# Kernel optimization log

Measured on AMD Instinct MI355X. Metric: run time of the kernel, lower is better.

The kernel has to match this reference:

```python
import jax, jax.numpy as jnp
import numpy as np

B, S, D, U = 64, 2048, 512, 512

def setup_inputs() -> dict:
    key = jax.random.key(0)
    ks = jax.random.split(key, 8)
    query = jax.random.normal(ks[0], (B, D), dtype=jnp.float32)
    values = jax.random.normal(ks[1], (B, S, D), dtype=jnp.float32)
    # Keras Dense params (glorot-like scale), with biases (Dense default use_bias=True)
    W1 = jax.random.normal(ks[2], (D, U), dtype=jnp.float32) / np.sqrt(D)
    b1 = jnp.zeros((U,), dtype=jnp.float32)
    W2 = jax.random.normal(ks[3], (D, U), dtype=jnp.float32) / np.sqrt(D)
    b2 = jnp.zeros((U,), dtype=jnp.float32)
    V = jax.random.normal(ks[4], (U, 1), dtype=jnp.float32) / np.sqrt(U)
    bv = jnp.zeros((1,), dtype=jnp.float32)
    return {"query": query, "values": values, "W1": W1, "b1": b1,
            "W2": W2, "b2": b2, "V": V, "bv": bv}

def reference(query, values, W1, b1, W2, b2, V, bv) -> jnp.ndarray:
    # query: [B, D], values: [B, S, D]
    q_proj = query @ W1 + b1                      # [B, U]
    v_proj = jnp.einsum('bsd,du->bsu', values, W2) + b2  # [B, S, U]
    h = jnp.tanh(q_proj[:, None, :] + v_proj)     # [B, S, U]
    scores = jnp.einsum('bsu,uo->bso', h, V) + bv # [B, S, 1]
    attn = jax.nn.softmax(scores, axis=1)         # softmax over sequence axis
    context = jnp.sum(attn * values, axis=1)      # [B, D]
    return context
```

## Files before the change

kernel.cpp:

```cpp
#include <hip/hip_runtime.h>
#include <hip/hip_bf16.h>

#define BB 64
#define SS 2048
#define DD 512
#define UU 512
#define BS (BB*SS)

typedef __attribute__((ext_vector_type(8))) short bf16x8;
typedef __attribute__((ext_vector_type(4))) float f32x4;

static __device__ __forceinline__ unsigned short f2bf(float x) {
    union { float f; unsigned int u; } v; v.f = x;
    unsigned int r = v.u + 0x7FFFu + ((v.u >> 16) & 1u);
    return (unsigned short)(r >> 16);
}

__global__ void k_w2t(const float* __restrict__ W2, unsigned short* __restrict__ W2T) {
    __shared__ float tile[64][65];
    const int ti = blockIdx.x >> 3;
    const int tj = blockIdx.x & 7;
    const int t = threadIdx.x;
    #pragma unroll
    for (int i = 0; i < 16; ++i) {
        int e = i*256 + t;
        int dr = e >> 6, uc = e & 63;
        tile[dr][uc] = W2[(size_t)(ti*64+dr)*UU + tj*64+uc];
    }
    __syncthreads();
    #pragma unroll
    for (int i = 0; i < 16; ++i) {
        int e = i*256 + t;
        int ur = e >> 6, dc = e & 63;
        W2T[(size_t)(tj*64+ur)*DD + ti*64+dc] = f2bf(tile[dc][ur]);
    }
}

__global__ void k_qproj(const float* __restrict__ query, const float* __restrict__ W1,
                        const float* __restrict__ b1, const float* __restrict__ b2,
                        float* __restrict__ qpb) {
    const int b = blockIdx.x, t = threadIdx.x;
    float a0 = 0.f, a1 = 0.f;
    for (int d = 0; d < DD; ++d) {
        float q = query[b*DD + d];
        a0 += q * W1[(size_t)d*UU + t];
        a1 += q * W1[(size_t)d*UU + t + 256];
    }
    qpb[b*UU + t]       = a0 + b1[t]     + b2[t];
    qpb[b*UU + t + 256] = a1 + b1[t+256] + b2[t+256];
}

__launch_bounds__(256, 2)
__global__ void k_scores(const float* __restrict__ values,
                         const unsigned short* __restrict__ W2T,
                         const float* __restrict__ qpb,
                         const float* __restrict__ Vw,
                         float* __restrict__ scores) {
    __shared__ unsigned short Albuf[64*512];
    const int t  = threadIdx.x;
    const int m0 = blockIdx.x * 64;
    const int b  = m0 >> 11;

    const float* src = values + (size_t)m0 * DD;
    #pragma unroll
    for (int i = 0; i < 16; ++i) {
        int gf  = i*256 + t;
        int row = gf >> 6;
        int g   = gf & 63;
        const float4 f0 = *(const float4*)(src + (size_t)row*DD + g*8);
        const float4 f1 = *(const float4*)(src + (size_t)row*DD + g*8 + 4);
        ushort4 lo, hi;
        lo.x = f2bf(f0.x); lo.y = f2bf(f0.y); lo.z = f2bf(f0.z); lo.w = f2bf(f0.w);
        hi.x = f2bf(f1.x); hi.y = f2bf(f1.y); hi.z = f2bf(f1.z); hi.w = f2bf(f1.w);
        int gs = g ^ (row & 7);
        ushort4* dst = (ushort4*)&Albuf[row*512 + gs*8];
        dst[0] = lo; dst[1] = hi;
    }
    __syncthreads();

    const int wave = t >> 6, lane = t & 63;
    const int ln15 = lane & 15, quad = lane >> 4;

    float sacc[4][4] = {};

    for (int nc = 0; nc < 2; ++nc) {
        const int nwb = nc*256 + wave*64;
        f32x4 acc[4][4];
        #pragma unroll
        for (int mt = 0; mt < 4; ++mt)
            #pragma unroll
            for (int nt = 0; nt < 4; ++nt)
                acc[mt][nt] = f32x4{0.f, 0.f, 0.f, 0.f};

        #pragma unroll 2
        for (int k0 = 0; k0 < DD; k0 += 32) {
            const int kq = k0 + quad*8;
            bf16x8 bfr[4], afr[4];
            #pragma unroll
            for (int nt = 0; nt < 4; ++nt) {
                int n = nwb + nt*16 + ln15;
                bfr[nt] = *(const bf16x8*)(W2T + (size_t)n*DD + kq);
            }
            #pragma unroll
            for (int mt = 0; mt < 4; ++mt) {
                int m = mt*16 + ln15;
                int g = (kq >> 3) ^ (m & 7);
                afr[mt] = *(const bf16x8*)&Albuf[m*512 + g*8];
            }
            #pragma unroll
            for (int mt = 0; mt < 4; ++mt)
                #pragma unroll
                for (int nt = 0; nt < 4; ++nt)
                    acc[mt][nt] = __builtin_amdgcn_mfma_f32_16x16x32_bf16(
                        afr[mt], bfr[nt], acc[mt][nt], 0, 0, 0);
        }

        #pragma unroll
        for (int nt = 0; nt < 4; ++nt) {
            int n = nwb + nt*16 + ln15;
            float qv = qpb[b*UU + n];
            float vw = Vw[n];
            #pragma unroll
            for (int mt = 0; mt < 4; ++mt)
                #pragma unroll
                for (int r = 0; r < 4; ++r) {
                    float x = qv + acc[mt][nt][r];
                    float e = __expf(x + x);
                    float h = 1.f - 2.f / (e + 1.f);
                    sacc[mt][r] += h * vw;
                }
        }
    }

    #pragma unroll
    for (int mt = 0; mt < 4; ++mt)
        #pragma unroll
        for (int r = 0; r < 4; ++r) {
            float v = sacc[mt][r];
            v += __shfl_xor(v, 1);
            v += __shfl_xor(v, 2);
            v += __shfl_xor(v, 4);
            v += __shfl_xor(v, 8);
            if (ln15 == 0)
                atomicAdd(&scores[m0 + mt*16 + quad*4 + r], v);
        }
}

__global__ void k_softmax(const float* __restrict__ scores, float* __restrict__ wts) {
    __shared__ float red[64];
    const int b = blockIdx.x, t = threadIdx.x;
    const float* s = scores + b*SS;
    float v[8];
    float mx = -1e30f;
    #pragma unroll
    for (int i = 0; i < 8; ++i) { v[i] = s[i*256 + t]; mx = fmaxf(mx, v[i]); }
    #pragma unroll
    for (int off = 32; off; off >>= 1) mx = fmaxf(mx, __shfl_xor(mx, off));
    if ((t & 63) == 0) red[t >> 6] = mx;
    __syncthreads();
    mx = fmaxf(fmaxf(red[0], red[1]), fmaxf(red[2], red[3]));
    float sum = 0.f;
    #pragma unroll
    for (int i = 0; i < 8; ++i) { v[i] = __expf(v[i] - mx); sum += v[i]; }
    #pragma unroll
    for (int off = 32; off; off >>= 1) sum += __shfl_xor(sum, off);
    __syncthreads();
    if ((t & 63) == 0) red[t >> 6] = sum;
    __syncthreads();
    sum = red[0] + red[1] + red[2] + red[3];
    float inv = 1.f / sum;
    #pragma unroll
    for (int i = 0; i < 8; ++i) wts[b*SS + i*256 + t] = v[i] * inv;
}

__launch_bounds__(256)
__global__ void k_context(const float* __restrict__ values, const float* __restrict__ wts,
                          float* __restrict__ out) {
    __shared__ float4 red[16][16];
    const int blk = blockIdx.x;
    const int b = blk >> 3, d0 = (blk & 7) * 64;
    const int t = threadIdx.x;
    const int di = t & 15, sg = t >> 4;
    float4 acc = make_float4(0.f, 0.f, 0.f, 0.f);
    const float* vb = values + (size_t)b*SS*DD + d0 + di*4;
    const float* wb = wts + b*SS;
    #pragma unroll 4
    for (int s = sg; s < SS; s += 16) {
        float w = wb[s];
        float4 v = *(const float4*)(vb + (size_t)s*DD);
        acc.x += w*v.x; acc.y += w*v.y; acc.z += w*v.z; acc.w += w*v.w;
    }
    red[sg][di] = acc;
    __syncthreads();
    if (t < 16) {
        float4 sum = make_float4(0.f, 0.f, 0.f, 0.f);
        #pragma unroll
        for (int g = 0; g < 16; ++g) {
            float4 v = red[g][t];
            sum.x += v.x; sum.y += v.y; sum.z += v.z; sum.w += v.w;
        }
        *(float4*)(out + (size_t)b*DD + d0 + t*4) = sum;
    }
}

extern "C" void kernel_launch(void* const* d_in, const int* in_sizes, int n_in,
                              void* d_out, int out_size, void* d_ws, size_t ws_size,
                              hipStream_t stream) {
    const float* query  = (const float*)d_in[0];
    const float* values = (const float*)d_in[1];
    const float* W1     = (const float*)d_in[2];
    const float* b1     = (const float*)d_in[3];
    const float* W2     = (const float*)d_in[4];
    const float* b2     = (const float*)d_in[5];
    const float* Vw     = (const float*)d_in[6];

    char* ws = (char*)d_ws;
    unsigned short* W2T = (unsigned short*)ws;
    float* qpb    = (float*)(ws + 524288);
    float* scores = (float*)(ws + 524288 + 131072);
    float* wts    = (float*)(ws + 524288 + 131072 + 524288);
    float* out    = (float*)d_out;

    hipMemsetAsync(scores, 0, BS * sizeof(float), stream);
    k_w2t<<<64, 256, 0, stream>>>(W2, W2T);
    k_qproj<<<BB, 256, 0, stream>>>(query, W1, b1, b2, qpb);
    k_scores<<<BS/64, 256, 0, stream>>>(values, W2T, qpb, Vw, scores);
    k_softmax<<<BB, 256, 0, stream>>>(scores, wts);
    k_context<<<BB*8, 256, 0, stream>>>(values, wts, out);
}
```

Baseline: 576.1 us.

## Merge prep kernels, fuse softmax into context, prefetch W2T, drop atomics

Merges the W2 transpose and query-projection kernels into one launch. Folds the softmax into the context kernel, so each block recomputes the per-batch softmax and keeps the weights in shared memory. In the scores kernel, W2T fragments are now double-buffered in registers and the per-column q/V constants are hoisted. The atomic score accumulation is replaced by a shared-memory reduction with a plain store, which removes the memset. Softmax work is repeated 8 times per batch, and register pressure in the scores kernel goes up.

```diff
diff --git a/kernel.cpp b/kernel.cpp
--- a/kernel.cpp
+++ b/kernel.cpp
@@ -16,38 +16,39 @@
     return (unsigned short)(r >> 16);
 }
 
-__global__ void k_w2t(const float* __restrict__ W2, unsigned short* __restrict__ W2T) {
+__global__ void k_prep(const float* __restrict__ W2, unsigned short* __restrict__ W2T,
+                       const float* __restrict__ query, const float* __restrict__ W1,
+                       const float* __restrict__ b1, const float* __restrict__ b2,
+                       float* __restrict__ qpb) {
     __shared__ float tile[64][65];
-    const int ti = blockIdx.x >> 3;
-    const int tj = blockIdx.x & 7;
     const int t = threadIdx.x;
-    #pragma unroll
-    for (int i = 0; i < 16; ++i) {
-        int e = i*256 + t;
-        int dr = e >> 6, uc = e & 63;
-        tile[dr][uc] = W2[(size_t)(ti*64+dr)*UU + tj*64+uc];
-    }
-    __syncthreads();
-    #pragma unroll
-    for (int i = 0; i < 16; ++i) {
-        int e = i*256 + t;
-        int ur = e >> 6, dc = e & 63;
-        W2T[(size_t)(tj*64+ur)*DD + ti*64+dc] = f2bf(tile[dc][ur]);
-    }
-}
-
-__global__ void k_qproj(const float* __restrict__ query, const float* __restrict__ W1,
-                        const float* __restrict__ b1, const float* __restrict__ b2,
-                        float* __restrict__ qpb) {
-    const int b = blockIdx.x, t = threadIdx.x;
-    float a0 = 0.f, a1 = 0.f;
-    for (int d = 0; d < DD; ++d) {
-        float q = query[b*DD + d];
-        a0 += q * W1[(size_t)d*UU + t];
-        a1 += q * W1[(size_t)d*UU + t + 256];
-    }
-    qpb[b*UU + t]       = a0 + b1[t]     + b2[t];
-    qpb[b*UU + t + 256] = a1 + b1[t+256] + b2[t+256];
+    if (blockIdx.x < 64) {
+        const int ti = blockIdx.x >> 3;
+        const int tj = blockIdx.x & 7;
+        #pragma unroll
+        for (int i = 0; i < 16; ++i) {
+            int e = i*256 + t;
+            int dr = e >> 6, uc = e & 63;
+            tile[dr][uc] = W2[(size_t)(ti*64+dr)*UU + tj*64+uc];
+        }
+        __syncthreads();
+        #pragma unroll
+        for (int i = 0; i < 16; ++i) {
+            int e = i*256 + t;
+            int ur = e >> 6, dc = e & 63;
+            W2T[(size_t)(tj*64+ur)*DD + ti*64+dc] = f2bf(tile[dc][ur]);
+        }
+    } else {
+        const int b = blockIdx.x - 64;
+        float a0 = 0.f, a1 = 0.f;
+        for (int d = 0; d < DD; ++d) {
+            float q = query[b*DD + d];
+            a0 += q * W1[(size_t)d*UU + t];
+            a1 += q * W1[(size_t)d*UU + t + 256];
+        }
+        qpb[b*UU + t]       = a0 + b1[t]     + b2[t];
+        qpb[b*UU + t + 256] = a1 + b1[t+256] + b2[t+256];
+    }
 }
 
 __launch_bounds__(256, 2)
@@ -60,6 +61,19 @@
     const int t  = threadIdx.x;
     const int m0 = blockIdx.x * 64;
     const int b  = m0 >> 11;
+
+    const int wave = t >> 6, lane = t & 63;
+    const int ln15 = lane & 15, quad = lane >> 4;
+
+    float qv[2][4], vw[2][4];
+    #pragma unroll
+    for (int nc = 0; nc < 2; ++nc)
+        #pragma unroll
+        for (int nt = 0; nt < 4; ++nt) {
+            int n = nc*256 + wave*64 + nt*16 + ln15;
+            qv[nc][nt] = qpb[b*UU + n];
+            vw[nc][nt] = Vw[n];
+        }
 
     const float* src = values + (size_t)m0 * DD;
     #pragma unroll
@@ -78,13 +92,25 @@
     }
     __syncthreads();
 
-    const int wave = t >> 6, lane = t & 63;
-    const int ln15 = lane & 15, quad = lane >> 4;
+    const unsigned short* bp[4];
+    #pragma unroll
+    for (int nt = 0; nt < 4; ++nt)
+        bp[nt] = W2T + (size_t)(wave*64 + nt*16 + ln15) * DD + quad*8;
+
+    int abase[4];
+    #pragma unroll
+    for (int mt = 0; mt < 4; ++mt)
+        abase[mt] = (mt*16 + ln15) * 512;
+    const int xm = ln15 & 7;
 
     float sacc[4][4] = {};
 
+    bf16x8 bb[2][4];
+    #pragma unroll
+    for (int nt = 0; nt < 4; ++nt)
+        bb[0][nt] = *(const bf16x8*)(bp[nt]);
+
     for (int nc = 0; nc < 2; ++nc) {
-        const int nwb = nc*256 + wave*64;
         f32x4 acc[4][4];
         #pragma unroll
         for (int mt = 0; mt < 4; ++mt)
@@ -92,46 +118,48 @@
             for (int nt = 0; nt < 4; ++nt)
                 acc[mt][nt] = f32x4{0.f, 0.f, 0.f, 0.f};
 
-        #pragma unroll 2
-        for (int k0 = 0; k0 < DD; k0 += 32) {
-            const int kq = k0 + quad*8;
-            bf16x8 bfr[4], afr[4];
-            #pragma unroll
-            for (int nt = 0; nt < 4; ++nt) {
-                int n = nwb + nt*16 + ln15;
-                bfr[nt] = *(const bf16x8*)(W2T + (size_t)n*DD + kq);
+        #pragma unroll
+        for (int ks = 0; ks < 16; ++ks) {
+            const int j   = nc*16 + ks;
+            const int cur = j & 1;
+            if (j + 1 < 32) {
+                const int jn  = j + 1;
+                const int off = (jn >> 4) * (256*DD) + (jn & 15) * 32;
+                #pragma unroll
+                for (int nt = 0; nt < 4; ++nt)
+                    bb[cur ^ 1][nt] = *(const bf16x8*)(bp[nt] + off);
             }
-            #pragma unroll
-            for (int mt = 0; mt < 4; ++mt) {
-                int m = mt*16 + ln15;
-                int g = (kq >> 3) ^ (m & 7);
-                afr[mt] = *(const bf16x8*)&Albuf[m*512 + g*8];
-            }
+            bf16x8 afr[4];
+            const int g4 = ks*4 + quad;
+            #pragma unroll
+            for (int mt = 0; mt < 4; ++mt)
+                afr[mt] = *(const bf16x8*)&Albuf[abase[mt] + ((g4 ^ xm) << 3)];
             #pragma unroll
             for (int mt = 0; mt < 4; ++mt)
                 #pragma unroll
                 for (int nt = 0; nt < 4; ++nt)
                     acc[mt][nt] = __builtin_amdgcn_mfma_f32_16x16x32_bf16(
-                        afr[mt], bfr[nt], acc[mt][nt], 0, 0, 0);
+                        afr[mt], bb[cur][nt], acc[mt][nt], 0, 0, 0);
         }
 
         #pragma unroll
         for (int nt = 0; nt < 4; ++nt) {
-            int n = nwb + nt*16 + ln15;
-            float qv = qpb[b*UU + n];
-            float vw = Vw[n];
+            const float q = qv[nc][nt];
+            const float w = vw[nc][nt];
             #pragma unroll
             for (int mt = 0; mt < 4; ++mt)
                 #pragma unroll
                 for (int r = 0; r < 4; ++r) {
-                    float x = qv + acc[mt][nt][r];
+                    float x = q + acc[mt][nt][r];
                     float e = __expf(x + x);
-                    float h = 1.f - 2.f / (e + 1.f);
-                    sacc[mt][r] += h * vw;
+                    float rc = __builtin_amdgcn_rcpf(e + 1.f);
+                    sacc[mt][r] = fmaf(fmaf(-2.f, rc, 1.f), w, sacc[mt][r]);
                 }
         }
     }
 
+    __syncthreads();
+    float* buf = (float*)Albuf;
     #pragma unroll
     for (int mt = 0; mt < 4; ++mt)
         #pragma unroll
@@ -141,65 +169,66 @@
             v += __shfl_xor(v, 2);
             v += __shfl_xor(v, 4);
             v += __shfl_xor(v, 8);
-            if (ln15 == 0)
-                atomicAdd(&scores[m0 + mt*16 + quad*4 + r], v);
-        }
-}
-
-__global__ void k_softmax(const float* __restrict__ scores, float* __restrict__ wts) {
-    __shared__ float red[64];
-    const int b = blockIdx.x, t = threadIdx.x;
-    const float* s = scores + b*SS;
-    float v[8];
-    float mx = -1e30f;
-    #pragma unroll
-    for (int i = 0; i < 8; ++i) { v[i] = s[i*256 + t]; mx = fmaxf(mx, v[i]); }
-    #pragma unroll
-    for (int off = 32; off; off >>= 1) mx = fmaxf(mx, __shfl_xor(mx, off));
-    if ((t & 63) == 0) red[t >> 6] = mx;
-    __syncthreads();
-    mx = fmaxf(fmaxf(red[0], red[1]), fmaxf(red[2], red[3]));
-    float sum = 0.f;
-    #pragma unroll
-    for (int i = 0; i < 8; ++i) { v[i] = __expf(v[i] - mx); sum += v[i]; }
-    #pragma unroll
-    for (int off = 32; off; off >>= 1) sum += __shfl_xor(sum, off);
-    __syncthreads();
-    if ((t & 63) == 0) red[t >> 6] = sum;
-    __syncthreads();
-    sum = red[0] + red[1] + red[2] + red[3];
-    float inv = 1.f / sum;
-    #pragma unroll
-    for (int i = 0; i < 8; ++i) wts[b*SS + i*256 + t] = v[i] * inv;
+            if (ln15 == 0) buf[wave*64 + mt*16 + quad*4 + r] = v;
+        }
+    __syncthreads();
+    if (t < 64)
+        scores[m0 + t] = buf[t] + buf[64 + t] + buf[128 + t] + buf[192 + t];
 }
 
 __launch_bounds__(256)
-__global__ void k_context(const float* __restrict__ values, const float* __restrict__ wts,
+__global__ void k_context(const float* __restrict__ values, const float* __restrict__ scores,
                           float* __restrict__ out) {
+    __shared__ float w[SS];
+    __shared__ float red8[8];
     __shared__ float4 red[16][16];
     const int blk = blockIdx.x;
     const int b = blk >> 3, d0 = (blk & 7) * 64;
     const int t = threadIdx.x;
+
+    const float* sc = scores + b*SS;
+    float v[8];
+    float mx = -1e30f;
+    #pragma unroll
+    for (int i = 0; i < 8; ++i) { v[i] = sc[i*256 + t]; mx = fmaxf(mx, v[i]); }
+    #pragma unroll
+    for (int off = 32; off; off >>= 1) mx = fmaxf(mx, __shfl_xor(mx, off));
+    if ((t & 63) == 0) red8[t >> 6] = mx;
+    __syncthreads();
+    mx = fmaxf(fmaxf(red8[0], red8[1]), fmaxf(red8[2], red8[3]));
+    float sum = 0.f;
+    #pragma unroll
+    for (int i = 0; i < 8; ++i) { v[i] = __expf(v[i] - mx); sum += v[i]; }
+    #pragma unroll
+    for (int off = 32; off; off >>= 1) sum += __shfl_xor(sum, off);
+    __syncthreads();
+    if ((t & 63) == 0) red8[4 + (t >> 6)] = sum;
+    __syncthreads();
+    sum = red8[4] + red8[5] + red8[6] + red8[7];
+    float inv = 1.f / sum;
+    #pragma unroll
+    for (int i = 0; i < 8; ++i) w[i*256 + t] = v[i] * inv;
+    __syncthreads();
+
     const int di = t & 15, sg = t >> 4;
     float4 acc = make_float4(0.f, 0.f, 0.f, 0.f);
     const float* vb = values + (size_t)b*SS*DD + d0 + di*4;
-    const float* wb = wts + b*SS;
-    #pragma unroll 4
+    #pragma unroll 8
     for (int s = sg; s < SS; s += 16) {
-        float w = wb[s];
-        float4 v = *(const float4*)(vb + (size_t)s*DD);
-        acc.x += w*v.x; acc.y += w*v.y; acc.z += w*v.z; acc.w += w*v.w;
+        float wgt = w[s];
+        float4 vv = *(const float4*)(vb + (size_t)s*DD);
+        acc.x += wgt*vv.x; acc.y += wgt*vv.y; acc.z += wgt*vv.z; acc.w += wgt*vv.w;
     }
     red[sg][di] = acc;
     __syncthreads();
     if (t < 16) {
-        float4 sum = make_float4(0.f, 0.f, 0.f, 0.f);
+        float4 s4 = make_float4(0.f, 0.f, 0.f, 0.f);
         #pragma unroll
         for (int g = 0; g < 16; ++g) {
-            float4 v = red[g][t];
-            sum.x += v.x; sum.y += v.y; sum.z += v.z; sum.w += v.w;
-        }
-        *(float4*)(out + (size_t)b*DD + d0 + t*4) = sum;
+            float4 vv = red[g][t];
+            s4.x += vv.x; s4.y += vv.y; s4.z += vv.z; s4.w += vv.w;
+        }
+        *(float4*)(out + (size_t)b*DD + d0 + t*4) = s4;
     }
 }
 
@@ -218,13 +247,9 @@
     unsigned short* W2T = (unsigned short*)ws;
     float* qpb    = (float*)(ws + 524288);
     float* scores = (float*)(ws + 524288 + 131072);
-    float* wts    = (float*)(ws + 524288 + 131072 + 524288);
     float* out    = (float*)d_out;
 
-    hipMemsetAsync(scores, 0, BS * sizeof(float), stream);
-    k_w2t<<<64, 256, 0, stream>>>(W2, W2T);
-    k_qproj<<<BB, 256, 0, stream>>>(query, W1, b1, b2, qpb);
+    k_prep<<<128, 256, 0, stream>>>(W2, W2T, query, W1, b1, b2, qpb);
     k_scores<<<BS/64, 256, 0, stream>>>(values, W2T, qpb, Vw, scores);
-    k_softmax<<<BB, 256, 0, stream>>>(scores, wts);
-    k_context<<<BB*8, 256, 0, stream>>>(values, wts, out);
-}
+    k_context<<<BB*8, 256, 0, stream>>>(values, scores, out);
+}
```

Result: no change. 585.0 us (+1.6%).
